# Kernel tuning notes

Measured on AMD Instinct MI355X. Metric: run time of the kernel, lower is better.

The kernel has to match this reference:

```python
import jax, jax.numpy as jnp
import numpy as np

BETA = 0.25
NUM_CODES = 512      # K
CODE_DIM = 64        # D (codebook_size)
N_TOKENS = 131072    # N


def setup_inputs() -> dict:
    key = jax.random.key(0)
    kx, kc = jax.random.split(key)
    x = jax.random.normal(kx, (N_TOKENS, CODE_DIM), dtype=jnp.float32)
    # keras 'random_uniform' initializer: U(-0.05, 0.05)
    codebook = jax.random.uniform(kc, (NUM_CODES, CODE_DIM), dtype=jnp.float32,
                                  minval=-0.05, maxval=0.05)
    return {"x": x, "codebook": codebook}


def reference(x, codebook):
    # Squared Euclidean distances [N, K] via expansion; argmin is identical
    # to argmin of tf.norm (sqrt is monotone).
    x2 = jnp.sum(x * x, axis=-1, keepdims=True)            # [N, 1]
    c2 = jnp.sum(codebook * codebook, axis=-1)             # [K]
    d2 = x2 - 2.0 * (x @ codebook.T) + c2[None, :]         # [N, K]
    indices = jnp.argmin(d2, axis=-1)                      # [N]
    quantized = jnp.take(codebook, indices, axis=0)        # [N, D]

    commitment_loss = jnp.mean((jax.lax.stop_gradient(quantized) - x) ** 2)
    codebook_loss = jnp.mean((quantized - jax.lax.stop_gradient(x)) ** 2)
    loss = BETA * commitment_loss + codebook_loss

    # straight-through estimator
    quantized_st = x + jax.lax.stop_gradient(quantized - x)
    return quantized_st, loss
```

## Files before the change

### kernel.cpp

```cpp
#include <hip/hip_runtime.h>

#define N_TOK 131072
#define K_CODES 512
#define DIM 64
#define MARGIN_S 5e-5f
#define LIST_CAP 30000

typedef __attribute__((ext_vector_type(8))) short bfx8;
typedef __attribute__((ext_vector_type(4))) float f32x4;
typedef __attribute__((ext_vector_type(4))) int i32x4;

__device__ __forceinline__ unsigned short f2bf_rn(float f) {
    unsigned u = __float_as_uint(f);
    unsigned r = (u + 0x7FFF + ((u >> 16) & 1)) >> 16;
    return (unsigned short)r;
}
__device__ __forceinline__ float bf2f(unsigned short h) {
    return __uint_as_float(((unsigned)h) << 16);
}

__device__ __forceinline__ float np_sumsq64(const float* v) {
    float r[8];
#pragma unroll
    for (int j = 0; j < 8; ++j) r[j] = __fmul_rn(v[j], v[j]);
#pragma unroll
    for (int i = 8; i < 64; i += 8) {
#pragma unroll
        for (int j = 0; j < 8; ++j)
            r[j] = __fadd_rn(r[j], __fmul_rn(v[i + j], v[i + j]));
    }
    return __fadd_rn(__fadd_rn(__fadd_rn(r[0], r[1]), __fadd_rn(r[2], r[3])),
                     __fadd_rn(__fadd_rn(r[4], r[5]), __fadd_rn(r[6], r[7])));
}

__global__ __launch_bounds__(64) void vq_prep(
    const float* __restrict__ cb, float* __restrict__ cnorm,
    float* __restrict__ c2h, unsigned short* __restrict__ cbh,
    unsigned short* __restrict__ cbl)
{
    int k = blockIdx.x * 64 + threadIdx.x;
    if (k >= K_CODES) return;
    float v[DIM];
#pragma unroll
    for (int d = 0; d < DIM; ++d) {
        float f = cb[k * DIM + d];
        v[d] = f;
        unsigned short h = f2bf_rn(f);
        cbh[k * DIM + d] = h;
        cbl[k * DIM + d] = f2bf_rn(__fsub_rn(f, bf2f(h)));
    }
    float c2 = np_sumsq64(v);
    cnorm[k] = c2;
    c2h[k] = __fmul_rn(0.5f, c2);
}

__global__ __attribute__((amdgpu_flat_work_group_size(256, 256),
                          amdgpu_waves_per_eu(2, 2)))
void vq_screen(
    const float* __restrict__ x, const float* __restrict__ cb,
    const unsigned short* __restrict__ cbh, const unsigned short* __restrict__ cbl,
    const float* __restrict__ c2h, float* __restrict__ out,
    double* __restrict__ loss_acc, int* __restrict__ counter,
    int* __restrict__ list, int cap)
{
    __shared__ bfx8 lds_h[128 * 8];
    __shared__ bfx8 lds_l[128 * 8];
    __shared__ float lds_c2[K_CODES];
    __shared__ double wsum[4];

    const int tid = threadIdx.x;
    const int wave = (blockIdx.x << 2) + (tid >> 6);
    const int lane = tid & 63;
    const int tokb = wave << 6;
    const int lrow = lane & 15;
    const int lgrp = lane >> 4;
    const int lcol = lrow;

    const float inf = __int_as_float(0x7f800000);

    if (tid < 128) ((float4*)lds_c2)[tid] = ((const float4*)c2h)[tid];

#define SPL(F, J, AH, AL) { unsigned short h_ = f2bf_rn(F); \
    (AH)[J] = (short)h_; (AL)[J] = (short)f2bf_rn(__fsub_rn(F, bf2f(h_))); }
#define LOADX(m) \
    bfx8 ah0_##m, al0_##m, ah1_##m, al1_##m; \
    { const float* xr = x + ((size_t)(tokb + (m) * 16 + lrow) << 6) + (lgrp << 3); \
      float4 f0 = *(const float4*)xr; \
      float4 f1 = *(const float4*)(xr + 4); \
      float4 f2 = *(const float4*)(xr + 32); \
      float4 f3 = *(const float4*)(xr + 36); \
      SPL(f0.x, 0, ah0_##m, al0_##m) SPL(f0.y, 1, ah0_##m, al0_##m) \
      SPL(f0.z, 2, ah0_##m, al0_##m) SPL(f0.w, 3, ah0_##m, al0_##m) \
      SPL(f1.x, 4, ah0_##m, al0_##m) SPL(f1.y, 5, ah0_##m, al0_##m) \
      SPL(f1.z, 6, ah0_##m, al0_##m) SPL(f1.w, 7, ah0_##m, al0_##m) \
      SPL(f2.x, 0, ah1_##m, al1_##m) SPL(f2.y, 1, ah1_##m, al1_##m) \
      SPL(f2.z, 2, ah1_##m, al1_##m) SPL(f2.w, 3, ah1_##m, al1_##m) \
      SPL(f3.x, 4, ah1_##m, al1_##m) SPL(f3.y, 5, ah1_##m, al1_##m) \
      SPL(f3.z, 6, ah1_##m, al1_##m) SPL(f3.w, 7, ah1_##m, al1_##m) }
    LOADX(0) LOADX(1) LOADX(2) LOADX(3)
#undef LOADX
#undef SPL

    f32x4 best0 = {inf, inf, inf, inf}, best1 = best0, best2 = best0, best3 = best0;
    f32x4 sec0 = best0, sec1 = best0, sec2 = best0, sec3 = best0;
    i32x4 idx0 = {0, 0, 0, 0}, idx1 = idx0, idx2 = idx0, idx3 = idx0;

    for (int ph = 0; ph < 4; ++ph) {
        __syncthreads();
        {
            const bfx8* gh = (const bfx8*)cbh + (ph << 10);
            const bfx8* gl = (const bfx8*)cbl + (ph << 10);
#pragma unroll
            for (int it = 0; it < 4; ++it) {
                int g = (it << 8) + tid;
                int code = g >> 3, slot = g & 7;
                int dst = (code << 3) + (slot ^ (code & 7));
                lds_h[dst] = gh[g];
                lds_l[dst] = gl[g];
            }
        }
        __syncthreads();

        int lr_c = lrow;
        int s0_c = lgrp ^ (lr_c & 7);
        bfx8 bh0 = lds_h[(lr_c << 3) + s0_c];
        bfx8 bh1 = lds_h[(lr_c << 3) + (s0_c ^ 4)];
        bfx8 bl0 = lds_l[(lr_c << 3) + s0_c];
        bfx8 bl1 = lds_l[(lr_c << 3) + (s0_c ^ 4)];
        float cn = lds_c2[(ph << 7) + lr_c];

#pragma unroll
        for (int ctl = 0; ctl < 8; ++ctl) {
            const int code = (ph << 7) + (ctl << 4) + lrow;
            bfx8 nh0 = bh0, nh1 = bh1, nl0 = bl0, nl1 = bl1;
            float cnn = cn;
            if (ctl < 7) {
                int lr_n = ((ctl + 1) << 4) + lrow;
                int s0_n = lgrp ^ (lr_n & 7);
                nh0 = lds_h[(lr_n << 3) + s0_n];
                nh1 = lds_h[(lr_n << 3) + (s0_n ^ 4)];
                nl0 = lds_l[(lr_n << 3) + s0_n];
                nl1 = lds_l[(lr_n << 3) + (s0_n ^ 4)];
                cnn = lds_c2[(ph << 7) + lr_n];
            }

#define MACC(m) \
            f32x4 accP##m = {0.f, 0.f, 0.f, 0.f}; \
            f32x4 accQ##m = {0.f, 0.f, 0.f, 0.f}; \
            accP##m = __builtin_amdgcn_mfma_f32_16x16x32_bf16(ah0_##m, bh0, accP##m, 0, 0, 0); \
            accQ##m = __builtin_amdgcn_mfma_f32_16x16x32_bf16(ah1_##m, bh1, accQ##m, 0, 0, 0); \
            accP##m = __builtin_amdgcn_mfma_f32_16x16x32_bf16(al0_##m, bh0, accP##m, 0, 0, 0); \
            accQ##m = __builtin_amdgcn_mfma_f32_16x16x32_bf16(al1_##m, bh1, accQ##m, 0, 0, 0); \
            accP##m = __builtin_amdgcn_mfma_f32_16x16x32_bf16(ah0_##m, bl0, accP##m, 0, 0, 0); \
            accQ##m = __builtin_amdgcn_mfma_f32_16x16x32_bf16(ah1_##m, bl1, accQ##m, 0, 0, 0);
            MACC(0) MACC(1) MACC(2) MACC(3)
#undef MACC

#define UPD1(m, R) { float s = cn - (accP##m[R] + accQ##m[R]); \
            bool p = s < best##m[R]; \
            sec##m[R] = p ? best##m[R] : fminf(sec##m[R], s); \
            best##m[R] = p ? s : best##m[R]; \
            idx##m[R] = p ? code : idx##m[R]; }
#define UPDM(m) UPD1(m, 0) UPD1(m, 1) UPD1(m, 2) UPD1(m, 3)
            UPDM(0) UPDM(1) UPDM(2) UPDM(3)
#undef UPDM
#undef UPD1

            bh0 = nh0; bh1 = nh1; bl0 = nl0; bl1 = nl1; cn = cnn;
        }
    }

    i32x4 pk0, pk1, pk2, pk3;
#define REDR(m, R) { float b = best##m[R], sc = sec##m[R]; int ix = idx##m[R]; \
    _Pragma("unroll") \
    for (int off = 1; off < 16; off <<= 1) { \
        float ob = __shfl_xor(b, off, 64); \
        float os = __shfl_xor(sc, off, 64); \
        int   oi = __shfl_xor(ix, off, 64); \
        bool take = (ob < b) || (ob == b && oi < ix); \
        float ns = take ? fminf(b, os) : fminf(sc, ob); \
        b = take ? ob : b; ix = take ? oi : ix; sc = ns; } \
    pk##m[R] = ix | (((sc - b) < MARGIN_S) ? (1 << 30) : 0); }
#define REDM(m) REDR(m, 0) REDR(m, 1) REDR(m, 2) REDR(m, 3)
    REDM(0) REDM(1) REDM(2) REDM(3)
#undef REDM
#undef REDR

    double ls = 0.0;
#define EPI1(m, R) { int fi = pk##m[R]; \
    int bidx_t = fi & 0xFFFF; \
    int t = tokb + (m) * 16 + (lgrp << 2) + (R); \
    float4 xv = *((const float4*)(x + ((size_t)t << 6)) + lcol); \
    float4 qv = *((const float4*)(cb + ((size_t)bidx_t << 6)) + lcol); \
    float4 ov; \
    float e0 = __fsub_rn(qv.x, xv.x); ov.x = __fadd_rn(xv.x, e0); \
    float e1 = __fsub_rn(qv.y, xv.y); ov.y = __fadd_rn(xv.y, e1); \
    float e2 = __fsub_rn(qv.z, xv.z); ov.z = __fadd_rn(xv.z, e2); \
    float e3 = __fsub_rn(qv.w, xv.w); ov.w = __fadd_rn(xv.w, e3); \
    *((float4*)(out + ((size_t)t << 6)) + lcol) = ov; \
    if (!(fi >> 30)) \
        ls += (double)e0 * e0 + (double)e1 * e1 + (double)e2 * e2 + (double)e3 * e3; \
    else if (lcol == 0) { int pos = atomicAdd(counter, 1); \
                          if (pos < cap) list[pos] = t; } }
#define EPIM(m) EPI1(m, 0) EPI1(m, 1) EPI1(m, 2) EPI1(m, 3)
    EPIM(0) EPIM(1) EPIM(2) EPIM(3)
#undef EPIM
#undef EPI1

#pragma unroll
    for (int off = 32; off > 0; off >>= 1) ls += __shfl_down(ls, off, 64);
    if (lane == 0) wsum[tid >> 6] = ls;
    __syncthreads();
    if (tid == 0)
        atomicAdd(loss_acc, (wsum[0] + wsum[1]) + (wsum[2] + wsum[3]));
}

#define RERANK_BLOCKS 256
__global__ __launch_bounds__(256) void vq_rerank(
    const float* __restrict__ x, const float* __restrict__ cb,
    const float* __restrict__ cnorm, float* __restrict__ out,
    double* __restrict__ loss_acc, const int* __restrict__ counter,
    const int* __restrict__ list, int cap,
    int* __restrict__ done, float* __restrict__ out_loss)
{
    int cnt = *counter; if (cnt > cap) cnt = cap;
    const int lane = threadIdx.x & 63;
    const int wid = (blockIdx.x << 2) + (threadIdx.x >> 6);
    const int nw = RERANK_BLOCKS << 2;
    double ls = 0.0;

    for (int i = wid; i < cnt; i += nw) {
        const int t = list[i];
        float xr[DIM];
        {
            const float4* xv = (const float4*)(x + ((size_t)t << 6));
#pragma unroll
            for (int q = 0; q < 16; ++q) {
                float4 v = xv[q];
                xr[4 * q + 0] = v.x; xr[4 * q + 1] = v.y;
                xr[4 * q + 2] = v.z; xr[4 * q + 3] = v.w;
            }
        }
        const float x2 = np_sumsq64(xr);
        float best = __int_as_float(0x7f800000);
        int bi = 0;
#pragma unroll 2
        for (int j = 0; j < 8; ++j) {
            const int k = (j << 6) + lane;
            const float4* c = (const float4*)(cb + ((size_t)k << 6));
            float a = 0.f;
#pragma unroll
            for (int q = 0; q < 16; ++q) {
                float4 f = c[q];
                a = __fmaf_rn(xr[4 * q + 0], f.x, a);
                a = __fmaf_rn(xr[4 * q + 1], f.y, a);
                a = __fmaf_rn(xr[4 * q + 2], f.z, a);
                a = __fmaf_rn(xr[4 * q + 3], f.w, a);
            }
            float d2 = __fadd_rn(__fsub_rn(x2, __fmul_rn(2.0f, a)), cnorm[k]);
            bool p = d2 < best;
            best = p ? d2 : best; bi = p ? k : bi;
        }
#pragma unroll
        for (int off = 1; off < 64; off <<= 1) {
            float ob = __shfl_xor(best, off, 64);
            int   oi = __shfl_xor(bi, off, 64);
            bool take = (ob < best) || (ob == best && oi < bi);
            best = take ? ob : best; bi = take ? oi : bi;
        }
        float xv = x[((size_t)t << 6) + lane];
        float q  = cb[((size_t)bi << 6) + lane];
        float e = __fsub_rn(q, xv);
        out[((size_t)t << 6) + lane] = __fadd_rn(xv, e);
        ls += (double)e * (double)e;
    }
#pragma unroll
    for (int off = 32; off > 0; off >>= 1) ls += __shfl_down(ls, off, 64);
    __shared__ double wsum[4];
    if (lane == 0) wsum[threadIdx.x >> 6] = ls;
    __syncthreads();
    if (threadIdx.x == 0) {
        double tot = (wsum[0] + wsum[1]) + (wsum[2] + wsum[3]);
        if (tot != 0.0) atomicAdd(loss_acc, tot);
        __threadfence();
        int prev = atomicAdd(done, 1);
        if (prev == RERANK_BLOCKS - 1) {
            __threadfence();
            double total = atomicAdd(loss_acc, 0.0);
            double mean = total / (double)((size_t)N_TOK * DIM);
            *out_loss = (float)(1.25 * mean);
        }
    }
}

extern "C" void kernel_launch(void* const* d_in, const int* in_sizes, int n_in,
                              void* d_out, int out_size, void* d_ws, size_t ws_size,
                              hipStream_t stream) {
    const float* x  = (const float*)d_in[0];
    const float* cb = (const float*)d_in[1];
    float* out = (float*)d_out;
    float* out_loss = out + (size_t)N_TOK * DIM;

    char* ws = (char*)d_ws;
    double* loss_acc = (double*)ws;
    int* counter = (int*)(ws + 8);
    int* done = (int*)(ws + 12);
    float* cnorm = (float*)(ws + 64);
    float* c2h = (float*)(ws + 2112);
    unsigned short* cbh = (unsigned short*)(ws + 4608);
    unsigned short* cbl = (unsigned short*)(ws + 70144);
    int* list = (int*)(ws + 135680);

    hipMemsetAsync(d_ws, 0, 32, stream);
    vq_prep<<<8, 64, 0, stream>>>(cb, cnorm, c2h, cbh, cbl);
    vq_screen<<<N_TOK / 256, 256, 0, stream>>>(x, cb, cbh, cbl, c2h, out,
                                               loss_acc, counter, list, LIST_CAP);
    vq_rerank<<<RERANK_BLOCKS, 256, 0, stream>>>(x, cb, cnorm, out, loss_acc,
                                                 counter, list, LIST_CAP,
                                                 done, out_loss);
}
```

Baseline: 83.65 us.

## Add transposed float4 codebook and two-token-per-wave rerank kernel

The prep kernel now stages the codebook through shared memory for coalesced loads, and optionally writes a transposed float4 codebook layout into the workspace. A new rerank kernel uses that layout so each lane holds eight codes and scores two flagged tokens per wave with FMA accumulators, followed by a joint butterfly argmin reduction. The intent is to cut the cost of the exact fp32 rerank of ambiguous tokens through coalesced codebook reads and reuse of each loaded code across two tokens. The new path only runs when the workspace is large enough, otherwise the old rerank kernel is used. The fma-based dot product may round differently from the previous path's summation order.

```diff
diff --git a/kernel.cpp b/kernel.cpp
--- a/kernel.cpp
+++ b/kernel.cpp
@@ -36,22 +36,40 @@
 __global__ __launch_bounds__(64) void vq_prep(
     const float* __restrict__ cb, float* __restrict__ cnorm,
     float* __restrict__ c2h, unsigned short* __restrict__ cbh,
-    unsigned short* __restrict__ cbl)
+    unsigned short* __restrict__ cbl, float4* __restrict__ cbT4)
 {
-    int k = blockIdx.x * 64 + threadIdx.x;
-    if (k >= K_CODES) return;
-    float v[DIM];
-#pragma unroll
-    for (int d = 0; d < DIM; ++d) {
-        float f = cb[k * DIM + d];
-        v[d] = f;
-        unsigned short h = f2bf_rn(f);
-        cbh[k * DIM + d] = h;
-        cbl[k * DIM + d] = f2bf_rn(__fsub_rn(f, bf2f(h)));
-    }
-    float c2 = np_sumsq64(v);
+    __shared__ float tile[64][65];
+    const int t = threadIdx.x;
+    const int b = blockIdx.x;
+    const float* src = cb + ((size_t)b << 12);
+
+#pragma unroll 4
+    for (int r = 0; r < 64; ++r)
+        tile[r][t] = src[(r << 6) + t];
+    __syncthreads();
+
+    const int k = (b << 6) + t;
+    float c2 = np_sumsq64(&tile[t][0]);
     cnorm[k] = c2;
     c2h[k] = __fmul_rn(0.5f, c2);
+
+#pragma unroll 4
+    for (int r = 0; r < 64; ++r) {
+        float f = tile[r][t];
+        unsigned short h = f2bf_rn(f);
+        cbh[((size_t)b << 12) + (r << 6) + t] = h;
+        cbl[((size_t)b << 12) + (r << 6) + t] = f2bf_rn(__fsub_rn(f, bf2f(h)));
+    }
+
+    if (cbT4) {
+#pragma unroll
+        for (int g = 0; g < 16; ++g) {
+            float4 w;
+            w.x = tile[t][4 * g + 0]; w.y = tile[t][4 * g + 1];
+            w.z = tile[t][4 * g + 2]; w.w = tile[t][4 * g + 3];
+            cbT4[(g << 9) + k] = w;
+        }
+    }
 }
 
 __global__ __attribute__((amdgpu_flat_work_group_size(256, 256),
@@ -215,7 +233,108 @@
         atomicAdd(loss_acc, (wsum[0] + wsum[1]) + (wsum[2] + wsum[3]));
 }
 
-#define RERANK_BLOCKS 256
+__global__ __launch_bounds__(256) void vq_rerank_t(
+    const float* __restrict__ x, const float* __restrict__ cb,
+    const float4* __restrict__ cbT4, const float* __restrict__ cnorm,
+    float* __restrict__ out, double* __restrict__ loss_acc,
+    const int* __restrict__ counter, const int* __restrict__ list, int cap,
+    int* __restrict__ done, float* __restrict__ out_loss)
+{
+    int cnt = *counter; if (cnt > cap) cnt = cap;
+    const int lane = threadIdx.x & 63;
+    const int wid = (blockIdx.x << 2) + (threadIdx.x >> 6);
+    const int nw = gridDim.x << 2;
+    const float inf = __int_as_float(0x7f800000);
+    double ls = 0.0;
+
+    for (int base = wid << 1; base < cnt; base += (nw << 1)) {
+        const int t0 = list[base];
+        const bool has1 = (base + 1) < cnt;
+        const int t1 = list[has1 ? base + 1 : base];
+        const float* x0p = x + ((size_t)t0 << 6);
+        const float* x1p = x + ((size_t)t1 << 6);
+
+        const float x2_0 = np_sumsq64(x0p);
+        const float x2_1 = np_sumsq64(x1p);
+
+        float A0 = 0.f, A1 = 0.f, A2 = 0.f, A3 = 0.f,
+              A4 = 0.f, A5 = 0.f, A6 = 0.f, A7 = 0.f;
+        float B0 = 0.f, B1 = 0.f, B2 = 0.f, B3 = 0.f,
+              B4 = 0.f, B5 = 0.f, B6 = 0.f, B7 = 0.f;
+#pragma unroll
+        for (int g = 0; g < 16; ++g) {
+            float4 xa = *(const float4*)(x0p + (g << 2));
+            float4 xb = *(const float4*)(x1p + (g << 2));
+#define STEP(j) { float4 c = cbT4[(g << 9) + ((j) << 6) + lane]; \
+            A##j = __fmaf_rn(xa.x, c.x, A##j); \
+            A##j = __fmaf_rn(xa.y, c.y, A##j); \
+            A##j = __fmaf_rn(xa.z, c.z, A##j); \
+            A##j = __fmaf_rn(xa.w, c.w, A##j); \
+            B##j = __fmaf_rn(xb.x, c.x, B##j); \
+            B##j = __fmaf_rn(xb.y, c.y, B##j); \
+            B##j = __fmaf_rn(xb.z, c.z, B##j); \
+            B##j = __fmaf_rn(xb.w, c.w, B##j); }
+            STEP(0) STEP(1) STEP(2) STEP(3)
+            STEP(4) STEP(5) STEP(6) STEP(7)
+#undef STEP
+        }
+
+        float best0 = inf, best1 = inf;
+        int bi0 = 0, bi1 = 0;
+#define SEL(j) { int k = ((j) << 6) + lane; float cn = cnorm[k]; \
+        float d2a = __fadd_rn(__fsub_rn(x2_0, __fmul_rn(2.0f, A##j)), cn); \
+        bool pa = d2a < best0; best0 = pa ? d2a : best0; bi0 = pa ? k : bi0; \
+        float d2b = __fadd_rn(__fsub_rn(x2_1, __fmul_rn(2.0f, B##j)), cn); \
+        bool pb = d2b < best1; best1 = pb ? d2b : best1; bi1 = pb ? k : bi1; }
+        SEL(0) SEL(1) SEL(2) SEL(3) SEL(4) SEL(5) SEL(6) SEL(7)
+#undef SEL
+#pragma unroll
+        for (int off = 1; off < 64; off <<= 1) {
+            float ob = __shfl_xor(best0, off, 64);
+            int   oi = __shfl_xor(bi0, off, 64);
+            bool take = (ob < best0) || (ob == best0 && oi < bi0);
+            best0 = take ? ob : best0; bi0 = take ? oi : bi0;
+            float ob1 = __shfl_xor(best1, off, 64);
+            int   oi1 = __shfl_xor(bi1, off, 64);
+            bool t1k = (ob1 < best1) || (ob1 == best1 && oi1 < bi1);
+            best1 = t1k ? ob1 : best1; bi1 = t1k ? oi1 : bi1;
+        }
+
+        {
+            float xv = x0p[lane];
+            float q  = cb[((size_t)bi0 << 6) + lane];
+            float e = __fsub_rn(q, xv);
+            out[((size_t)t0 << 6) + lane] = __fadd_rn(xv, e);
+            ls += (double)e * (double)e;
+        }
+        if (has1) {
+            float xv = x1p[lane];
+            float q  = cb[((size_t)bi1 << 6) + lane];
+            float e = __fsub_rn(q, xv);
+            out[((size_t)t1 << 6) + lane] = __fadd_rn(xv, e);
+            ls += (double)e * (double)e;
+        }
+    }
+
+#pragma unroll
+    for (int off = 32; off > 0; off >>= 1) ls += __shfl_down(ls, off, 64);
+    __shared__ double wsum[4];
+    if (lane == 0) wsum[threadIdx.x >> 6] = ls;
+    __syncthreads();
+    if (threadIdx.x == 0) {
+        double tot = (wsum[0] + wsum[1]) + (wsum[2] + wsum[3]);
+        if (tot != 0.0) atomicAdd(loss_acc, tot);
+        __threadfence();
+        int prev = atomicAdd(done, 1);
+        if (prev == (int)gridDim.x - 1) {
+            __threadfence();
+            double total = atomicAdd(loss_acc, 0.0);
+            double mean = total / (double)((size_t)N_TOK * DIM);
+            *out_loss = (float)(1.25 * mean);
+        }
+    }
+}
+
 __global__ __launch_bounds__(256) void vq_rerank(
     const float* __restrict__ x, const float* __restrict__ cb,
     const float* __restrict__ cnorm, float* __restrict__ out,
@@ -226,7 +345,7 @@
     int cnt = *counter; if (cnt > cap) cnt = cap;
     const int lane = threadIdx.x & 63;
     const int wid = (blockIdx.x << 2) + (threadIdx.x >> 6);
-    const int nw = RERANK_BLOCKS << 2;
+    const int nw = gridDim.x << 2;
     double ls = 0.0;
 
     for (int i = wid; i < cnt; i += nw) {
@@ -284,7 +403,7 @@
         if (tot != 0.0) atomicAdd(loss_acc, tot);
         __threadfence();
         int prev = atomicAdd(done, 1);
-        if (prev == RERANK_BLOCKS - 1) {
+        if (prev == (int)gridDim.x - 1) {
             __threadfence();
             double total = atomicAdd(loss_acc, 0.0);
             double mean = total / (double)((size_t)N_TOK * DIM);
@@ -309,13 +428,21 @@
     float* c2h = (float*)(ws + 2112);
     unsigned short* cbh = (unsigned short*)(ws + 4608);
     unsigned short* cbl = (unsigned short*)(ws + 70144);
-    int* list = (int*)(ws + 135680);
+
+    const bool big = ws_size >= (size_t)(266752 + LIST_CAP * 4 + 64);
+    float4* cbT4 = big ? (float4*)(ws + 135680) : nullptr;
+    int* list = (int*)(ws + (big ? 266752 : 135680));
 
     hipMemsetAsync(d_ws, 0, 32, stream);
-    vq_prep<<<8, 64, 0, stream>>>(cb, cnorm, c2h, cbh, cbl);
+    vq_prep<<<8, 64, 0, stream>>>(cb, cnorm, c2h, cbh, cbl, cbT4);
     vq_screen<<<N_TOK / 256, 256, 0, stream>>>(x, cb, cbh, cbl, c2h, out,
                                                loss_acc, counter, list, LIST_CAP);
-    vq_rerank<<<RERANK_BLOCKS, 256, 0, stream>>>(x, cb, cnorm, out, loss_acc,
-                                                 counter, list, LIST_CAP,
-                                                 done, out_loss);
-}
+    if (big)
+        vq_rerank_t<<<128, 256, 0, stream>>>(x, cb, cbT4, cnorm, out, loss_acc,
+                                             counter, list, LIST_CAP,
+                                             done, out_loss);
+    else
+        vq_rerank<<<256, 256, 0, stream>>>(x, cb, cnorm, out, loss_acc,
+                                           counter, list, LIST_CAP,
+                                           done, out_loss);
+}
```

Result: slower. 145.1 us (+73.4%).
